# Optimization experiments

Hardware: AMD Instinct MI355X
Metric: run time of the kernel (lower is better)

## Reference

```python
import jax, jax.numpy as jnp
import numpy as np
import math

S, B, D, H, NL, K = 64, 1024, 512, 8, 4, 32
DH = D // H
DFF = 4 * D


def _pe():
    # sinusoidal positional encoding, shape [S, 1, D], scaled by 1/sqrt(D)
    pos = np.arange(S, dtype=np.float32)[:, None]
    div = np.exp(np.arange(0, D, 2, dtype=np.float32) * (-math.log(10000.0) / D))
    pe = np.zeros((S, D), dtype=np.float32)
    pe[:, 0::2] = np.sin(pos * div)
    pe[:, 1::2] = np.cos(pos * div)
    return jnp.asarray(pe[:, None, :] / math.sqrt(D))


def _ln(x, g, b, eps=1e-5):
    m = jnp.mean(x, axis=-1, keepdims=True)
    v = jnp.mean(jnp.square(x - m), axis=-1, keepdims=True)
    return (x - m) * jax.lax.rsqrt(v + eps) * g + b


def setup_inputs() -> dict:
    key = jax.random.key(0)
    ks = jax.random.split(key, 16)
    s = 0.02
    return {
        "x": jax.random.normal(ks[0], (S, B, D), dtype=jnp.float32),
        "ln1_g": jnp.ones((NL, D), jnp.float32),
        "ln1_b": jnp.zeros((NL, D), jnp.float32),
        "qkv_w": jax.random.normal(ks[1], (NL, 3 * D, D), jnp.float32) * s,
        "qkv_b": jnp.zeros((NL, 3 * D), jnp.float32),
        "out_w": jax.random.normal(ks[2], (NL, D, D), jnp.float32) * s,
        "out_b": jnp.zeros((NL, D), jnp.float32),
        "ln2_g": jnp.ones((NL, D), jnp.float32),
        "ln2_b": jnp.zeros((NL, D), jnp.float32),
        "mlp_w1": jax.random.normal(ks[3], (NL, DFF, D), jnp.float32) * s,
        "mlp_b1": jnp.zeros((NL, DFF), jnp.float32),
        "mlp_w2": jax.random.normal(ks[4], (NL, D, DFF), jnp.float32) * s,
        "mlp_b2": jnp.zeros((NL, D), jnp.float32),
        "hash_w": jax.random.normal(ks[5], (K, D), jnp.float32) * s,
        "hash_b": jnp.zeros((K,), jnp.float32),
    }


def reference(x, ln1_g, ln1_b, qkv_w, qkv_b, out_w, out_b,
              ln2_g, ln2_b, mlp_w1, mlp_b1, mlp_w2, mlp_b2,
              hash_w, hash_b):
    # positional encoding (dropout p=0.0 is identity)
    x = x + _pe()
    scale = 1.0 / math.sqrt(DH)
    for i in range(NL):
        # pre-LN multi-head self-attention
        h = _ln(x, ln1_g[i], ln1_b[i])
        qkv = h @ qkv_w[i].T + qkv_b[i]                      # [S,B,3D]
        q, k, v = jnp.split(qkv, 3, axis=-1)
        q = q.reshape(S, B, H, DH)
        k = k.reshape(S, B, H, DH)
        v = v.reshape(S, B, H, DH)
        scores = jnp.einsum('sbhd,tbhd->bhst', q, k) * scale  # [B,H,S,S]
        attn = jax.nn.softmax(scores, axis=-1)
        o = jnp.einsum('bhst,tbhd->sbhd', attn, v).reshape(S, B, D)
        x = x + o @ out_w[i].T + out_b[i]
        # pre-LN MLP with QuickGELU
        h = _ln(x, ln2_g[i], ln2_b[i])
        h1 = h @ mlp_w1[i].T + mlp_b1[i]
        h1 = h1 * jax.nn.sigmoid(1.702 * h1)
        x = x + h1 @ mlp_w2[i].T + mlp_b2[i]
    # BitwiseHashing: per-bit Linear(D,1) applied per seq position, mean over S,
    # concat over k bits, tanh -> equals tanh(mean_S(x) @ W^T + b)
    pooled = jnp.mean(x, axis=0)                              # [B,D]
    return jnp.tanh(pooled @ hash_w.T + hash_b)               # [B,K]
```

## Files before the change

### kernel.cpp

```cpp
#include <hip/hip_runtime.h>
#include <hip/hip_bf16.h>
#include <math.h>

#define S_   64
#define B_   1024
#define D_   512
#define H_   8
#define NL_  4
#define DH_  64
#define DFF_ 2048
#define NTOK (S_*B_)

typedef __bf16 bf16;
typedef __bf16 bf16x8 __attribute__((ext_vector_type(8)));
typedef float  f32x4  __attribute__((ext_vector_type(4)));

#define AS1(p) ((__attribute__((address_space(1))) void*)(void*)(p))
#define AS3(p) ((__attribute__((address_space(3))) void*)(p))

__global__ __launch_bounds__(256) void cvt_k(const float* __restrict__ s,
                                             bf16* __restrict__ d, int n) {
    int i = (blockIdx.x * 256 + threadIdx.x) * 4;
    if (i < n) {
        float4 v = *(const float4*)(s + i);
        bf16 o4[4] = {(bf16)v.x, (bf16)v.y, (bf16)v.z, (bf16)v.w};
        *(ushort4*)(d + i) = *(const ushort4*)o4;
    }
}

__global__ __launch_bounds__(256) void pe_add_k(const float* __restrict__ x,
                                                float* __restrict__ X) {
    int id = blockIdx.x * 256 + threadIdx.x;
    int n = id >> 8;
    int j = id & 255;
    int s = n >> 10;
    float div = expf((float)j * -0.03597789207803197f);
    float ang = (float)s * div;
    const float inv = 0.04419417382415922f;
    float2 v = *(const float2*)(x + (long)n * 512 + 2 * j);
    v.x += sinf(ang) * inv;
    v.y += cosf(ang) * inv;
    *(float2*)(X + (long)n * 512 + 2 * j) = v;
}

__global__ __launch_bounds__(256) void ln_k(const float* __restrict__ X,
                                            const float* __restrict__ g,
                                            const float* __restrict__ be,
                                            bf16* __restrict__ out) {
    long row = (long)blockIdx.x * 4 + (threadIdx.x >> 6);
    int lane = threadIdx.x & 63;
    const float* xr = X + row * 512 + lane * 8;
    float4 v0 = *(const float4*)xr;
    float4 v1 = *(const float4*)(xr + 4);
    float vv[8] = {v0.x, v0.y, v0.z, v0.w, v1.x, v1.y, v1.z, v1.w};
    float s = 0.f, sq = 0.f;
    #pragma unroll
    for (int j = 0; j < 8; j++) { s += vv[j]; sq += vv[j] * vv[j]; }
    #pragma unroll
    for (int off = 1; off < 64; off <<= 1) {
        s  += __shfl_xor(s, off);
        sq += __shfl_xor(sq, off);
    }
    float mean = s * (1.f / 512.f);
    float var  = sq * (1.f / 512.f) - mean * mean;
    float rs = rsqrtf(var + 1e-5f);
    int d = lane * 8;
    bf16 o8[8];
    #pragma unroll
    for (int j = 0; j < 8; j++)
        o8[j] = (bf16)((vv[j] - mean) * rs * g[d + j] + be[d + j]);
    *(uint4*)(out + row * 512 + d) = *(const uint4*)o8;
}

template<int EPI>
__global__ __launch_bounds__(256)
void gemm_bt(const bf16* __restrict__ A, const bf16* __restrict__ Bw,
             const float* __restrict__ bias, float* __restrict__ Xres,
             bf16* __restrict__ Obf, int Mdim, int K) {
    __shared__ bf16 As[128 * 32];
    __shared__ bf16 Bs[128 * 32];
    const int tid  = threadIdx.x;
    const int lane = tid & 63;
    const int wave = tid >> 6;
    const long rowBlk = (long)blockIdx.y * 128;
    const long colBlk = (long)blockIdx.x * 128;

    const int c0 = tid;
    const bf16* ag0 = A  + (rowBlk + (c0 >> 2)) * K + (c0 & 3) * 8;
    const bf16* ag1 = ag0 + 64 * (long)K;
    const bf16* bg0 = Bw + (colBlk + (c0 >> 2)) * K + (c0 & 3) * 8;
    const bf16* bg1 = bg0 + 64 * (long)K;
    bf16* al0 = As + c0 * 8;
    bf16* al1 = As + (c0 + 256) * 8;
    bf16* bl0 = Bs + c0 * 8;
    bf16* bl1 = Bs + (c0 + 256) * 8;

    const int wm = (wave >> 1) * 64, wn = (wave & 1) * 64;
    const int lr = lane & 15, lq = lane >> 4;

    f32x4 acc[4][4] = {};

    for (int k0 = 0; k0 < K; k0 += 32) {
        __builtin_amdgcn_global_load_lds(AS1(ag0 + k0), AS3(al0), 16, 0, 0);
        __builtin_amdgcn_global_load_lds(AS1(ag1 + k0), AS3(al1), 16, 0, 0);
        __builtin_amdgcn_global_load_lds(AS1(bg0 + k0), AS3(bl0), 16, 0, 0);
        __builtin_amdgcn_global_load_lds(AS1(bg1 + k0), AS3(bl1), 16, 0, 0);
        __syncthreads();
        bf16x8 af[4], bfr[4];
        #pragma unroll
        for (int mi = 0; mi < 4; mi++)
            af[mi] = *(const bf16x8*)(As + (wm + mi * 16 + lr) * 32 + lq * 8);
        #pragma unroll
        for (int ni = 0; ni < 4; ni++)
            bfr[ni] = *(const bf16x8*)(Bs + (wn + ni * 16 + lr) * 32 + lq * 8);
        #pragma unroll
        for (int mi = 0; mi < 4; mi++)
            #pragma unroll
            for (int ni = 0; ni < 4; ni++)
                acc[mi][ni] = __builtin_amdgcn_mfma_f32_16x16x32_bf16(
                    af[mi], bfr[ni], acc[mi][ni], 0, 0, 0);
        __syncthreads();
    }

    #pragma unroll
    for (int mi = 0; mi < 4; mi++) {
        #pragma unroll
        for (int ni = 0; ni < 4; ni++) {
            #pragma unroll
            for (int r = 0; r < 4; r++) {
                long row = rowBlk + wm + mi * 16 + lq * 4 + r;
                long col = colBlk + wn + ni * 16 + lr;
                float v = acc[mi][ni][r] + bias[col];
                if (EPI == 0) {
                    Obf[row * Mdim + col] = (bf16)v;
                } else {
                    Xres[row * Mdim + col] += v;
                }
            }
        }
    }
}

__global__ __launch_bounds__(256, 2)
void fused_mlp(const bf16* __restrict__ A,
               const bf16* __restrict__ W1,
               const float* __restrict__ b1,
               const bf16* __restrict__ W2,
               const float* __restrict__ b2,
               float* __restrict__ X) {
    __shared__ bf16 As[64 * 128];
    __shared__ bf16 Ws[16384];
    __shared__ bf16 h1s[64 * 136];
    const int tid = threadIdx.x;
    const int lane = tid & 63;
    const int w = tid >> 6;
    const int lr = lane & 15, lq = lane >> 4;
    const long rowBlk = (long)blockIdx.x * 64;

    f32x4 acc2[4][8] = {};

    for (int j = 0; j < 16; j++) {
        f32x4 acc1[4][2] = {};
        for (int kk = 0; kk < 4; kk++) {
            #pragma unroll
            for (int r = 0; r < 4; r++) {
                int c = tid + r * 256;
                int row = c >> 4, ks = c & 15;
                int ko = ks ^ (row & 7);
                __builtin_amdgcn_global_load_lds(
                    AS1(A + (rowBlk + row) * 512 + kk * 128 + ko * 8),
                    AS3(As + c * 8), 16, 0, 0);
            }
            #pragma unroll
            for (int r = 0; r < 8; r++) {
                int c = tid + r * 256;
                int n = c >> 4, ks = c & 15;
                int ko = ks ^ (n & 7);
                __builtin_amdgcn_global_load_lds(
                    AS1(W1 + ((long)j * 128 + n) * 512 + kk * 128 + ko * 8),
                    AS3(Ws + c * 8), 16, 0, 0);
            }
            __syncthreads();
            #pragma unroll
            for (int kh = 0; kh < 4; kh++) {
                bf16x8 af[4], bfx[2];
                #pragma unroll
                for (int ri = 0; ri < 4; ri++) {
                    int row = ri * 16 + lr;
                    int ks = (kh * 4 + lq) ^ (row & 7);
                    af[ri] = *(const bf16x8*)(As + row * 128 + ks * 8);
                }
                #pragma unroll
                for (int ci = 0; ci < 2; ci++) {
                    int n = w * 32 + ci * 16 + lr;
                    int ks = (kh * 4 + lq) ^ (n & 7);
                    bfx[ci] = *(const bf16x8*)(Ws + n * 128 + ks * 8);
                }
                #pragma unroll
                for (int ri = 0; ri < 4; ri++)
                    #pragma unroll
                    for (int ci = 0; ci < 2; ci++)
                        acc1[ri][ci] = __builtin_amdgcn_mfma_f32_16x16x32_bf16(
                            af[ri], bfx[ci], acc1[ri][ci], 0, 0, 0);
            }
            __syncthreads();
        }
        #pragma unroll
        for (int ci = 0; ci < 2; ci++) {
            int col = w * 32 + ci * 16 + lr;
            float bv = b1[j * 128 + col];
            #pragma unroll
            for (int ri = 0; ri < 4; ri++) {
                #pragma unroll
                for (int r = 0; r < 4; r++) {
                    int row = ri * 16 + lq * 4 + r;
                    float v = acc1[ri][ci][r] + bv;
                    float g = v / (1.f + __expf(-1.702f * v));
                    h1s[row * 136 + col] = (bf16)g;
                }
            }
        }
        __syncthreads();
        for (int kk2 = 0; kk2 < 4; kk2++) {
            #pragma unroll
            for (int r = 0; r < 8; r++) {
                int c = tid + r * 256;
                int n = c >> 2, ks = c & 3;
                int ko = ks ^ ((n >> 1) & 3);
                __builtin_amdgcn_global_load_lds(
                    AS1(W2 + (long)n * 2048 + j * 128 + kk2 * 32 + ko * 8),
                    AS3(Ws + c * 8), 16, 0, 0);
            }
            __syncthreads();
            bf16x8 af2[4], bf2[8];
            #pragma unroll
            for (int ri = 0; ri < 4; ri++)
                af2[ri] = *(const bf16x8*)(h1s + (ri * 16 + lr) * 136 + kk2 * 32 + lq * 8);
            #pragma unroll
            for (int ci = 0; ci < 8; ci++) {
                int n = w * 128 + ci * 16 + lr;
                int ks = lq ^ ((n >> 1) & 3);
                bf2[ci] = *(const bf16x8*)(Ws + n * 32 + ks * 8);
            }
            #pragma unroll
            for (int ri = 0; ri < 4; ri++)
                #pragma unroll
                for (int ci = 0; ci < 8; ci++)
                    acc2[ri][ci] = __builtin_amdgcn_mfma_f32_16x16x32_bf16(
                        af2[ri], bf2[ci], acc2[ri][ci], 0, 0, 0);
            __syncthreads();
        }
    }
    #pragma unroll
    for (int ci = 0; ci < 8; ci++) {
        int col = w * 128 + ci * 16 + lr;
        float bv = b2[col];
        #pragma unroll
        for (int ri = 0; ri < 4; ri++) {
            #pragma unroll
            for (int r = 0; r < 4; r++) {
                long row = rowBlk + ri * 16 + lq * 4 + r;
                X[row * 512 + col] += acc2[ri][ci][r] + bv;
            }
        }
    }
}

__global__ __launch_bounds__(256)
void attn_k(const bf16* __restrict__ qkv, bf16* __restrict__ o) {
    __shared__ bf16 qs[64 * 64], ks[64 * 64], vts[64 * 64], ps[64 * 64];
    const int tid = threadIdx.x;
    const int b = blockIdx.x >> 3;
    const int h = blockIdx.x & 7;
    const int lane = tid & 63;
    const int w = tid >> 6;

    #pragma unroll
    for (int half = 0; half < 2; half++) {
        int c = tid + half * 256;
        int trow = c >> 3;
        int off = (c & 7) * 8;
        const bf16* base = qkv + ((long)(trow * B_ + b)) * 1536 + h * 64 + off;
        *(uint4*)(qs + trow * 64 + off) = *(const uint4*)(base);
        *(uint4*)(ks + trow * 64 + off) = *(const uint4*)(base + 512);
        uint4 vv = *(const uint4*)(base + 1024);
        bf16 vtmp[8];
        *(uint4*)vtmp = vv;
        #pragma unroll
        for (int j = 0; j < 8; j++) vts[(off + j) * 64 + trow] = vtmp[j];
    }
    __syncthreads();

    const int lr = lane & 15, lq = lane >> 4;

    f32x4 sc[4] = {};
    #pragma unroll
    for (int d0 = 0; d0 < 64; d0 += 32) {
        bf16x8 aq = *(const bf16x8*)(qs + (w * 16 + lr) * 64 + d0 + lq * 8);
        #pragma unroll
        for (int ni = 0; ni < 4; ni++) {
            bf16x8 bk = *(const bf16x8*)(ks + (ni * 16 + lr) * 64 + d0 + lq * 8);
            sc[ni] = __builtin_amdgcn_mfma_f32_16x16x32_bf16(aq, bk, sc[ni], 0, 0, 0);
        }
    }
    float p[4][4];
    #pragma unroll
    for (int r = 0; r < 4; r++) {
        float m = -1e30f;
        #pragma unroll
        for (int ni = 0; ni < 4; ni++) { sc[ni][r] *= 0.125f; m = fmaxf(m, sc[ni][r]); }
        #pragma unroll
        for (int off = 1; off < 16; off <<= 1) m = fmaxf(m, __shfl_xor(m, off));
        float sum = 0.f;
        #pragma unroll
        for (int ni = 0; ni < 4; ni++) { p[ni][r] = __expf(sc[ni][r] - m); sum += p[ni][r]; }
        #pragma unroll
        for (int off = 1; off < 16; off <<= 1) sum += __shfl_xor(sum, off);
        float inv = 1.f / sum;
        #pragma unroll
        for (int ni = 0; ni < 4; ni++)
            ps[(w * 16 + lq * 4 + r) * 64 + ni * 16 + lr] = (bf16)(p[ni][r] * inv);
    }
    __syncthreads();

    f32x4 oa[4] = {};
    #pragma unroll
    for (int t0 = 0; t0 < 64; t0 += 32) {
        bf16x8 ap = *(const bf16x8*)(ps + (w * 16 + lr) * 64 + t0 + lq * 8);
        #pragma unroll
        for (int ni = 0; ni < 4; ni++) {
            bf16x8 bv = *(const bf16x8*)(vts + (ni * 16 + lr) * 64 + t0 + lq * 8);
            oa[ni] = __builtin_amdgcn_mfma_f32_16x16x32_bf16(ap, bv, oa[ni], 0, 0, 0);
        }
    }
    #pragma unroll
    for (int ni = 0; ni < 4; ni++) {
        #pragma unroll
        for (int r = 0; r < 4; r++) {
            int s = w * 16 + lq * 4 + r;
            int d = ni * 16 + lr;
            o[((long)(s * B_ + b)) * 512 + h * 64 + d] = (bf16)oa[ni][r];
        }
    }
}

__global__ __launch_bounds__(256)
void poolhash_k(const float* __restrict__ X, const float* __restrict__ hw,
                const float* __restrict__ hb, float* __restrict__ out) {
    __shared__ float pooled[512];
    __shared__ float part[8][32];
    int b = blockIdx.x, tid = threadIdx.x;
    for (int d = tid; d < 512; d += 256) {
        float acc = 0.f;
        #pragma unroll 8
        for (int s = 0; s < 64; s++) acc += X[((long)(s * B_ + b)) * 512 + d];
        pooled[d] = acc * (1.f / 64.f);
    }
    __syncthreads();
    int k = tid & 31, ch = tid >> 5;
    float p = 0.f;
    for (int d = ch * 64; d < ch * 64 + 64; d++) p += pooled[d] * hw[k * 512 + d];
    part[ch][k] = p;
    __syncthreads();
    if (tid < 32) {
        float t = hb[tid];
        #pragma unroll
        for (int c = 0; c < 8; c++) t += part[c][tid];
        out[b * 32 + tid] = tanhf(t);
    }
}

extern "C" void kernel_launch(void* const* d_in, const int* in_sizes, int n_in,
                              void* d_out, int out_size, void* d_ws, size_t ws_size,
                              hipStream_t stream) {
    const float* x      = (const float*)d_in[0];
    const float* ln1_g  = (const float*)d_in[1];
    const float* ln1_b  = (const float*)d_in[2];
    const float* qkv_w  = (const float*)d_in[3];
    const float* qkv_b  = (const float*)d_in[4];
    const float* out_w  = (const float*)d_in[5];
    const float* out_b  = (const float*)d_in[6];
    const float* ln2_g  = (const float*)d_in[7];
    const float* ln2_b  = (const float*)d_in[8];
    const float* mlp_w1 = (const float*)d_in[9];
    const float* mlp_b1 = (const float*)d_in[10];
    const float* mlp_w2 = (const float*)d_in[11];
    const float* mlp_b2 = (const float*)d_in[12];
    const float* hash_w = (const float*)d_in[13];
    const float* hash_b = (const float*)d_in[14];

    char* ws = (char*)d_ws;
    float* X  = (float*)ws;
    bf16* BIG = (bf16*)(ws + 134217728);
    bf16* Hb  = (bf16*)(ws + 134217728 + 268435456);
    size_t wo = 134217728 + 268435456 + 67108864;
    bf16* Wq = (bf16*)(ws + wo);            wo += (size_t)NL_ * 1536 * 512 * 2;
    bf16* Wo = (bf16*)(ws + wo);            wo += (size_t)NL_ * 512 * 512 * 2;
    bf16* W1 = (bf16*)(ws + wo);            wo += (size_t)NL_ * 2048 * 512 * 2;
    bf16* W2 = (bf16*)(ws + wo);            wo += (size_t)NL_ * 512 * 2048 * 2;

    cvt_k<<<(NL_ * 1536 * 512) / 1024, 256, 0, stream>>>(qkv_w,  Wq, NL_ * 1536 * 512);
    cvt_k<<<(NL_ * 512  * 512) / 1024, 256, 0, stream>>>(out_w,  Wo, NL_ * 512  * 512);
    cvt_k<<<(NL_ * 2048 * 512) / 1024, 256, 0, stream>>>(mlp_w1, W1, NL_ * 2048 * 512);
    cvt_k<<<(NL_ * 512 * 2048) / 1024, 256, 0, stream>>>(mlp_w2, W2, NL_ * 512 * 2048);

    pe_add_k<<<(NTOK * 256) / 256, 256, 0, stream>>>(x, X);

    for (int i = 0; i < NL_; i++) {
        ln_k<<<NTOK / 4, 256, 0, stream>>>(X, ln1_g + i * 512, ln1_b + i * 512, Hb);
        gemm_bt<0><<<dim3(12, 512), 256, 0, stream>>>(Hb, Wq + (size_t)i * 1536 * 512,
                                                      qkv_b + i * 1536, nullptr, BIG, 1536, 512);
        attn_k<<<B_ * H_, 256, 0, stream>>>(BIG, Hb);
        gemm_bt<2><<<dim3(4, 512), 256, 0, stream>>>(Hb, Wo + (size_t)i * 512 * 512,
                                                     out_b + i * 512, X, nullptr, 512, 512);
        ln_k<<<NTOK / 4, 256, 0, stream>>>(X, ln2_g + i * 512, ln2_b + i * 512, Hb);
        fused_mlp<<<NTOK / 64, 256, 0, stream>>>(Hb, W1 + (size_t)i * 2048 * 512,
                                                 mlp_b1 + i * 2048,
                                                 W2 + (size_t)i * 512 * 2048,
                                                 mlp_b2 + i * 512, X);
    }

    poolhash_k<<<B_, 256, 0, stream>>>(X, hash_w, hash_b, (float*)d_out);
}
```

Measured before the change: 3.742 ms.

## Split fused MLP over 8 waves and alias A and h1 LDS buffers

The fused MLP kernel moves from 4 to 8 waves per block. Each wave now owns a 2x2 tile of the first GEMM and a 64-column slice of the second GEMM, which halves the per-thread accumulator state. The A-tile and h1 staging buffers share one LDS region, cutting LDS per block and removing one barrier. The aim is higher occupancy and more latency hiding. The aggressive launch bound (512 threads, 4 blocks) may force the compiler to cap registers, which risks spills, and LDS capacity may still limit resident blocks.

```diff
diff --git a/kernel.cpp b/kernel.cpp
--- a/kernel.cpp
+++ b/kernel.cpp
@@ -141,39 +141,39 @@
     }
 }
 
-__global__ __launch_bounds__(256, 2)
+__global__ __launch_bounds__(512, 4)
 void fused_mlp(const bf16* __restrict__ A,
                const bf16* __restrict__ W1,
                const float* __restrict__ b1,
                const bf16* __restrict__ W2,
                const float* __restrict__ b2,
                float* __restrict__ X) {
-    __shared__ bf16 As[64 * 128];
+    __shared__ bf16 U[8704];
     __shared__ bf16 Ws[16384];
-    __shared__ bf16 h1s[64 * 136];
     const int tid = threadIdx.x;
     const int lane = tid & 63;
     const int w = tid >> 6;
     const int lr = lane & 15, lq = lane >> 4;
     const long rowBlk = (long)blockIdx.x * 64;
-
-    f32x4 acc2[4][8] = {};
+    const int mh = w & 1, nq = w >> 1;
+
+    f32x4 acc2[4][4] = {};
 
     for (int j = 0; j < 16; j++) {
-        f32x4 acc1[4][2] = {};
+        f32x4 acc1[2][2] = {};
         for (int kk = 0; kk < 4; kk++) {
             #pragma unroll
-            for (int r = 0; r < 4; r++) {
-                int c = tid + r * 256;
+            for (int r = 0; r < 2; r++) {
+                int c = tid + r * 512;
                 int row = c >> 4, ks = c & 15;
                 int ko = ks ^ (row & 7);
                 __builtin_amdgcn_global_load_lds(
                     AS1(A + (rowBlk + row) * 512 + kk * 128 + ko * 8),
-                    AS3(As + c * 8), 16, 0, 0);
-            }
-            #pragma unroll
-            for (int r = 0; r < 8; r++) {
-                int c = tid + r * 256;
+                    AS3(U + c * 8), 16, 0, 0);
+            }
+            #pragma unroll
+            for (int r = 0; r < 4; r++) {
+                int c = tid + r * 512;
                 int n = c >> 4, ks = c & 15;
                 int ko = ks ^ (n & 7);
                 __builtin_amdgcn_global_load_lds(
@@ -183,48 +183,46 @@
             __syncthreads();
             #pragma unroll
             for (int kh = 0; kh < 4; kh++) {
-                bf16x8 af[4], bfx[2];
+                int g = kh * 4 + lq;
+                bf16x8 af[2], bfx[2];
                 #pragma unroll
-                for (int ri = 0; ri < 4; ri++) {
-                    int row = ri * 16 + lr;
-                    int ks = (kh * 4 + lq) ^ (row & 7);
-                    af[ri] = *(const bf16x8*)(As + row * 128 + ks * 8);
+                for (int mi = 0; mi < 2; mi++) {
+                    int row = mh * 32 + mi * 16 + lr;
+                    af[mi] = *(const bf16x8*)(U + row * 128 + (g ^ (row & 7)) * 8);
                 }
                 #pragma unroll
-                for (int ci = 0; ci < 2; ci++) {
-                    int n = w * 32 + ci * 16 + lr;
-                    int ks = (kh * 4 + lq) ^ (n & 7);
-                    bfx[ci] = *(const bf16x8*)(Ws + n * 128 + ks * 8);
+                for (int ni = 0; ni < 2; ni++) {
+                    int n = nq * 32 + ni * 16 + lr;
+                    bfx[ni] = *(const bf16x8*)(Ws + n * 128 + (g ^ (n & 7)) * 8);
                 }
                 #pragma unroll
-                for (int ri = 0; ri < 4; ri++)
+                for (int mi = 0; mi < 2; mi++)
                     #pragma unroll
-                    for (int ci = 0; ci < 2; ci++)
-                        acc1[ri][ci] = __builtin_amdgcn_mfma_f32_16x16x32_bf16(
-                            af[ri], bfx[ci], acc1[ri][ci], 0, 0, 0);
+                    for (int ni = 0; ni < 2; ni++)
+                        acc1[mi][ni] = __builtin_amdgcn_mfma_f32_16x16x32_bf16(
+                            af[mi], bfx[ni], acc1[mi][ni], 0, 0, 0);
             }
             __syncthreads();
         }
         #pragma unroll
-        for (int ci = 0; ci < 2; ci++) {
-            int col = w * 32 + ci * 16 + lr;
+        for (int ni = 0; ni < 2; ni++) {
+            int col = nq * 32 + ni * 16 + lr;
             float bv = b1[j * 128 + col];
             #pragma unroll
-            for (int ri = 0; ri < 4; ri++) {
+            for (int mi = 0; mi < 2; mi++) {
                 #pragma unroll
                 for (int r = 0; r < 4; r++) {
-                    int row = ri * 16 + lq * 4 + r;
-                    float v = acc1[ri][ci][r] + bv;
-                    float g = v / (1.f + __expf(-1.702f * v));
-                    h1s[row * 136 + col] = (bf16)g;
+                    int row = mh * 32 + mi * 16 + lq * 4 + r;
+                    float v = acc1[mi][ni][r] + bv;
+                    float gv = v / (1.f + __expf(-1.702f * v));
+                    U[row * 136 + col] = (bf16)gv;
                 }
             }
         }
-        __syncthreads();
         for (int kk2 = 0; kk2 < 4; kk2++) {
             #pragma unroll
-            for (int r = 0; r < 8; r++) {
-                int c = tid + r * 256;
+            for (int r = 0; r < 4; r++) {
+                int c = tid + r * 512;
                 int n = c >> 2, ks = c & 3;
                 int ko = ks ^ ((n >> 1) & 3);
                 __builtin_amdgcn_global_load_lds(
@@ -232,35 +230,34 @@
                     AS3(Ws + c * 8), 16, 0, 0);
             }
             __syncthreads();
-            bf16x8 af2[4], bf2[8];
+            bf16x8 af2[4], bf2[4];
             #pragma unroll
             for (int ri = 0; ri < 4; ri++)
-                af2[ri] = *(const bf16x8*)(h1s + (ri * 16 + lr) * 136 + kk2 * 32 + lq * 8);
-            #pragma unroll
-            for (int ci = 0; ci < 8; ci++) {
-                int n = w * 128 + ci * 16 + lr;
-                int ks = lq ^ ((n >> 1) & 3);
-                bf2[ci] = *(const bf16x8*)(Ws + n * 32 + ks * 8);
+                af2[ri] = *(const bf16x8*)(U + (ri * 16 + lr) * 136 + kk2 * 32 + lq * 8);
+            #pragma unroll
+            for (int ni = 0; ni < 4; ni++) {
+                int n = w * 64 + ni * 16 + lr;
+                bf2[ni] = *(const bf16x8*)(Ws + n * 32 + ((lq ^ ((n >> 1) & 3))) * 8);
             }
             #pragma unroll
             for (int ri = 0; ri < 4; ri++)
                 #pragma unroll
-                for (int ci = 0; ci < 8; ci++)
-                    acc2[ri][ci] = __builtin_amdgcn_mfma_f32_16x16x32_bf16(
-                        af2[ri], bf2[ci], acc2[ri][ci], 0, 0, 0);
+                for (int ni = 0; ni < 4; ni++)
+                    acc2[ri][ni] = __builtin_amdgcn_mfma_f32_16x16x32_bf16(
+                        af2[ri], bf2[ni], acc2[ri][ni], 0, 0, 0);
             __syncthreads();
         }
     }
     #pragma unroll
-    for (int ci = 0; ci < 8; ci++) {
-        int col = w * 128 + ci * 16 + lr;
+    for (int ni = 0; ni < 4; ni++) {
+        int col = w * 64 + ni * 16 + lr;
         float bv = b2[col];
         #pragma unroll
         for (int ri = 0; ri < 4; ri++) {
             #pragma unroll
             for (int r = 0; r < 4; r++) {
                 long row = rowBlk + ri * 16 + lq * 4 + r;
-                X[row * 512 + col] += acc2[ri][ci][r] + bv;
+                X[row * 512 + col] += acc2[ri][ni][r] + bv;
             }
         }
     }
@@ -414,7 +411,7 @@
         gemm_bt<2><<<dim3(4, 512), 256, 0, stream>>>(Hb, Wo + (size_t)i * 512 * 512,
                                                      out_b + i * 512, X, nullptr, 512, 512);
         ln_k<<<NTOK / 4, 256, 0, stream>>>(X, ln2_g + i * 512, ln2_b + i * 512, Hb);
-        fused_mlp<<<NTOK / 64, 256, 0, stream>>>(Hb, W1 + (size_t)i * 2048 * 512,
+        fused_mlp<<<NTOK / 64, 512, 0, stream>>>(Hb, W1 + (size_t)i * 2048 * 512,
                                                  mlp_b1 + i * 2048,
                                                  W2 + (size_t)i * 512 * 2048,
                                                  mlp_b2 + i * 512, X);
```

Measured after the change: 4.192 ms. 1.12x slower.

## Double-buffer weights and switch fused MLP to 32x32x16 MFMA with fragment-ordered LDS

Applied to the files above, without the earlier changes.

Rewrites the fused MLP kernel to use 32x32x16 bf16 MFMA instead of 16x16x32, stages A, W1 and W2 into LDS in a fragment-native layout so each lane reads contiguous 16-byte chunks without swizzle math, and double-buffers the weight tiles so the next W1/W2 tile loads while the current one is multiplied. The h1 activation tile reuses the A staging buffer. The intent is to hide global-to-LDS latency and cut LDS read instructions per MFMA. In exchange, shared memory use and synchronisation ordering grow more complex, and the buffer reuse carries a risk of races.

```diff
diff --git a/kernel.cpp b/kernel.cpp
--- a/kernel.cpp
+++ b/kernel.cpp
@@ -14,6 +14,7 @@
 typedef __bf16 bf16;
 typedef __bf16 bf16x8 __attribute__((ext_vector_type(8)));
 typedef float  f32x4  __attribute__((ext_vector_type(4)));
+typedef float  f32x16 __attribute__((ext_vector_type(16)));
 
 #define AS1(p) ((__attribute__((address_space(1))) void*)(void*)(p))
 #define AS3(p) ((__attribute__((address_space(3))) void*)(p))
@@ -148,119 +149,132 @@
                const bf16* __restrict__ W2,
                const float* __restrict__ b2,
                float* __restrict__ X) {
-    __shared__ bf16 As[64 * 128];
-    __shared__ bf16 Ws[16384];
-    __shared__ bf16 h1s[64 * 136];
-    const int tid = threadIdx.x;
+    __shared__ bf16 U[8192];
+    __shared__ bf16 Wb[2][16384];
+    const int tid  = threadIdx.x;
     const int lane = tid & 63;
-    const int w = tid >> 6;
-    const int lr = lane & 15, lq = lane >> 4;
+    const int w    = tid >> 6;
+    const int lh   = lane >> 5;
+    const int l31  = lane & 31;
     const long rowBlk = (long)blockIdx.x * 64;
-
-    f32x4 acc2[4][8] = {};
+    const int mh    = w & 1;
+    const int cpair = (w >> 1) * 2;
+
+    auto stageA = [&](int kk) {
+        #pragma unroll
+        for (int r = 0; r < 4; r++) {
+            int c = tid + r * 256;
+            int mt = c >> 9, s = (c >> 6) & 7, l = c & 63;
+            __builtin_amdgcn_global_load_lds(
+                AS1(A + (rowBlk + mt * 32 + (l & 31)) * 512
+                      + kk * 128 + s * 16 + (l >> 5) * 8),
+                AS3(U + c * 8), 16, 0, 0);
+        }
+    };
+    auto stageW1 = [&](int j, int kk, int pb) {
+        #pragma unroll
+        for (int r = 0; r < 8; r++) {
+            int c = tid + r * 256;
+            int nt1 = c >> 9, s = (c >> 6) & 7, l = c & 63;
+            __builtin_amdgcn_global_load_lds(
+                AS1(W1 + ((long)j * 128 + nt1 * 32 + (l & 31)) * 512
+                      + kk * 128 + s * 16 + (l >> 5) * 8),
+                AS3(Wb[pb] + c * 8), 16, 0, 0);
+        }
+    };
+    auto stageW2 = [&](int j, int kk2, int pb) {
+        #pragma unroll
+        for (int r = 0; r < 8; r++) {
+            int c = tid + r * 256;
+            int nt = c >> 7, s3 = (c >> 6) & 1, l = c & 63;
+            __builtin_amdgcn_global_load_lds(
+                AS1(W2 + ((long)(nt * 32 + (l & 31))) * 2048
+                      + j * 128 + kk2 * 32 + s3 * 16 + (l >> 5) * 8),
+                AS3(Wb[pb] + c * 8), 16, 0, 0);
+        }
+    };
+
+    f32x16 acc2[2][4] = {};
+
+    stageW1(0, 0, 0);
 
     for (int j = 0; j < 16; j++) {
-        f32x4 acc1[4][2] = {};
+        f32x16 acc1[2] = {};
         for (int kk = 0; kk < 4; kk++) {
-            #pragma unroll
-            for (int r = 0; r < 4; r++) {
-                int c = tid + r * 256;
-                int row = c >> 4, ks = c & 15;
-                int ko = ks ^ (row & 7);
-                __builtin_amdgcn_global_load_lds(
-                    AS1(A + (rowBlk + row) * 512 + kk * 128 + ko * 8),
-                    AS3(As + c * 8), 16, 0, 0);
-            }
-            #pragma unroll
-            for (int r = 0; r < 8; r++) {
-                int c = tid + r * 256;
-                int n = c >> 4, ks = c & 15;
-                int ko = ks ^ (n & 7);
-                __builtin_amdgcn_global_load_lds(
-                    AS1(W1 + ((long)j * 128 + n) * 512 + kk * 128 + ko * 8),
-                    AS3(Ws + c * 8), 16, 0, 0);
-            }
             __syncthreads();
-            #pragma unroll
-            for (int kh = 0; kh < 4; kh++) {
-                bf16x8 af[4], bfx[2];
+            stageA(kk);
+            __syncthreads();
+            if (kk < 3) stageW1(j, kk + 1, (kk + 1) & 1);
+            else        stageW2(j, 0, 0);
+            const bf16* Wp = Wb[kk & 1];
+            #pragma unroll
+            for (int s = 0; s < 8; s++) {
+                bf16x8 af = *(const bf16x8*)(U + ((mh * 8 + s) * 64 + lane) * 8);
                 #pragma unroll
-                for (int ri = 0; ri < 4; ri++) {
-                    int row = ri * 16 + lr;
-                    int ks = (kh * 4 + lq) ^ (row & 7);
-                    af[ri] = *(const bf16x8*)(As + row * 128 + ks * 8);
+                for (int ct = 0; ct < 2; ct++) {
+                    bf16x8 bfr = *(const bf16x8*)
+                        (Wp + (((cpair + ct) * 8 + s) * 64 + lane) * 8);
+                    acc1[ct] = __builtin_amdgcn_mfma_f32_32x32x16_bf16(
+                        af, bfr, acc1[ct], 0, 0, 0);
                 }
-                #pragma unroll
-                for (int ci = 0; ci < 2; ci++) {
-                    int n = w * 32 + ci * 16 + lr;
-                    int ks = (kh * 4 + lq) ^ (n & 7);
-                    bfx[ci] = *(const bf16x8*)(Ws + n * 128 + ks * 8);
-                }
-                #pragma unroll
-                for (int ri = 0; ri < 4; ri++)
-                    #pragma unroll
-                    for (int ci = 0; ci < 2; ci++)
-                        acc1[ri][ci] = __builtin_amdgcn_mfma_f32_16x16x32_bf16(
-                            af[ri], bfx[ci], acc1[ri][ci], 0, 0, 0);
-            }
-            __syncthreads();
-        }
-        #pragma unroll
-        for (int ci = 0; ci < 2; ci++) {
-            int col = w * 32 + ci * 16 + lr;
-            float bv = b1[j * 128 + col];
-            #pragma unroll
-            for (int ri = 0; ri < 4; ri++) {
-                #pragma unroll
-                for (int r = 0; r < 4; r++) {
-                    int row = ri * 16 + lq * 4 + r;
-                    float v = acc1[ri][ci][r] + bv;
-                    float g = v / (1.f + __expf(-1.702f * v));
-                    h1s[row * 136 + col] = (bf16)g;
-                }
-            }
-        }
+            }
+        }
+        __syncthreads();
+        #pragma unroll
+        for (int ct = 0; ct < 2; ct++) {
+            int colg = (cpair + ct) * 32 + l31;
+            float b1v = b1[j * 128 + colg];
+            bf16* dst = U + (mh * 8 + (colg >> 4)) * 512
+                          + ((colg >> 3) & 1) * 256 + (colg & 7);
+            #pragma unroll
+            for (int r = 0; r < 16; r++) {
+                int rowin = (r & 3) + 8 * (r >> 2) + 4 * lh;
+                float v = acc1[ct][r] + b1v;
+                float gv = v / (1.f + __expf(-1.702f * v));
+                dst[rowin * 8] = (bf16)gv;
+            }
+        }
+        stageW2(j, 1, 1);
         __syncthreads();
         for (int kk2 = 0; kk2 < 4; kk2++) {
-            #pragma unroll
-            for (int r = 0; r < 8; r++) {
-                int c = tid + r * 256;
-                int n = c >> 2, ks = c & 3;
-                int ko = ks ^ ((n >> 1) & 3);
-                __builtin_amdgcn_global_load_lds(
-                    AS1(W2 + (long)n * 2048 + j * 128 + kk2 * 32 + ko * 8),
-                    AS3(Ws + c * 8), 16, 0, 0);
-            }
-            __syncthreads();
-            bf16x8 af2[4], bf2[8];
-            #pragma unroll
-            for (int ri = 0; ri < 4; ri++)
-                af2[ri] = *(const bf16x8*)(h1s + (ri * 16 + lr) * 136 + kk2 * 32 + lq * 8);
-            #pragma unroll
-            for (int ci = 0; ci < 8; ci++) {
-                int n = w * 128 + ci * 16 + lr;
-                int ks = lq ^ ((n >> 1) & 3);
-                bf2[ci] = *(const bf16x8*)(Ws + n * 32 + ks * 8);
-            }
-            #pragma unroll
-            for (int ri = 0; ri < 4; ri++)
+            const bf16* Wp = Wb[kk2 & 1];
+            #pragma unroll
+            for (int s3 = 0; s3 < 2; s3++) {
+                int sblk = kk2 * 2 + s3;
+                bf16x8 af2[2], bf2[4];
                 #pragma unroll
-                for (int ci = 0; ci < 8; ci++)
-                    acc2[ri][ci] = __builtin_amdgcn_mfma_f32_16x16x32_bf16(
-                        af2[ri], bf2[ci], acc2[ri][ci], 0, 0, 0);
-            __syncthreads();
-        }
-    }
-    #pragma unroll
-    for (int ci = 0; ci < 8; ci++) {
-        int col = w * 128 + ci * 16 + lr;
+                for (int m2 = 0; m2 < 2; m2++)
+                    af2[m2] = *(const bf16x8*)
+                        (U + ((m2 * 8 + sblk) * 64 + lane) * 8);
+                #pragma unroll
+                for (int ci = 0; ci < 4; ci++)
+                    bf2[ci] = *(const bf16x8*)
+                        (Wp + (((w * 4 + ci) * 2 + s3) * 64 + lane) * 8);
+                #pragma unroll
+                for (int m2 = 0; m2 < 2; m2++)
+                    #pragma unroll
+                    for (int ci = 0; ci < 4; ci++)
+                        acc2[m2][ci] = __builtin_amdgcn_mfma_f32_32x32x16_bf16(
+                            af2[m2], bf2[ci], acc2[m2][ci], 0, 0, 0);
+            }
+            if (kk2 < 3) {
+                __syncthreads();
+                if      (kk2 == 0) stageW2(j, 2, 0);
+                else if (kk2 == 1) stageW2(j, 3, 1);
+                else if (j < 15)   stageW1(j + 1, 0, 0);
+            }
+        }
+    }
+    #pragma unroll
+    for (int ci = 0; ci < 4; ci++) {
+        int col = w * 128 + ci * 32 + l31;
         float bv = b2[col];
         #pragma unroll
-        for (int ri = 0; ri < 4; ri++) {
-            #pragma unroll
-            for (int r = 0; r < 4; r++) {
-                long row = rowBlk + ri * 16 + lq * 4 + r;
-                X[row * 512 + col] += acc2[ri][ci][r] + bv;
+        for (int m2 = 0; m2 < 2; m2++) {
+            #pragma unroll
+            for (int r = 0; r < 16; r++) {
+                long row = rowBlk + m2 * 32 + (r & 3) + 8 * (r >> 2) + 4 * lh;
+                X[row * 512 + col] += acc2[m2][ci][r] + bv;
             }
         }
     }
```

Result: slower. 5.533 ms (+47.8%).

## Double-buffer fused MLP LDS tiles to overlap global loads with MFMA

Applied to the files above, without the earlier changes.

Restructures the fused MLP kernel to use two LDS buffers with smaller K chunks (64 for GEMM1, half-N chunks for GEMM2), prefetching the next stage's tiles, including across the GEMM1/GEMM2 boundary and into the next j iteration, while computing on the current one. This removes the load-then-sync stall at each K step. It also remaps the W2 column assignment so each wave covers interleaved 16-column groups. Halving the chunk size doubles the number of barriers, and the LDS footprint stays about the same, so occupancy should be unchanged.

```diff
diff --git a/kernel.cpp b/kernel.cpp
--- a/kernel.cpp
+++ b/kernel.cpp
@@ -148,53 +148,72 @@
                const bf16* __restrict__ W2,
                const float* __restrict__ b2,
                float* __restrict__ X) {
-    __shared__ bf16 As[64 * 128];
-    __shared__ bf16 Ws[16384];
+    __shared__ bf16 As[2][4096];
+    __shared__ bf16 Ws[2][8192];
     __shared__ bf16 h1s[64 * 136];
-    const int tid = threadIdx.x;
+    const int tid  = threadIdx.x;
     const int lane = tid & 63;
-    const int w = tid >> 6;
+    const int w    = tid >> 6;
     const int lr = lane & 15, lq = lane >> 4;
     const long rowBlk = (long)blockIdx.x * 64;
 
+    auto stage1 = [&](int j, int c, int pb) {
+        #pragma unroll
+        for (int r = 0; r < 2; r++) {
+            int cc = tid + r * 256;
+            int row = cc >> 3, ks = cc & 7;
+            int ko = ks ^ (row & 7);
+            __builtin_amdgcn_global_load_lds(
+                AS1(A + (rowBlk + row) * 512 + c * 64 + ko * 8),
+                AS3(As[pb] + cc * 8), 16, 0, 0);
+        }
+        #pragma unroll
+        for (int r = 0; r < 4; r++) {
+            int cc = tid + r * 256;
+            int n = cc >> 3, ks = cc & 7;
+            int ko = ks ^ (n & 7);
+            __builtin_amdgcn_global_load_lds(
+                AS1(W1 + ((long)j * 128 + n) * 512 + c * 64 + ko * 8),
+                AS3(Ws[pb] + cc * 8), 16, 0, 0);
+        }
+    };
+    auto stage2 = [&](int j, int c, int pb) {
+        int kc = c >> 1, nh = c & 1;
+        #pragma unroll
+        for (int r = 0; r < 4; r++) {
+            int cc = tid + r * 256;
+            int n = cc >> 2, ks = cc & 3;
+            int ko = ks ^ ((n >> 1) & 3);
+            __builtin_amdgcn_global_load_lds(
+                AS1(W2 + ((long)(nh * 256 + n)) * 2048 + j * 128 + kc * 32 + ko * 8),
+                AS3(Ws[pb] + cc * 8), 16, 0, 0);
+        }
+    };
+
     f32x4 acc2[4][8] = {};
+
+    stage1(0, 0, 0);
+    __syncthreads();
 
     for (int j = 0; j < 16; j++) {
         f32x4 acc1[4][2] = {};
-        for (int kk = 0; kk < 4; kk++) {
-            #pragma unroll
-            for (int r = 0; r < 4; r++) {
-                int c = tid + r * 256;
-                int row = c >> 4, ks = c & 15;
-                int ko = ks ^ (row & 7);
-                __builtin_amdgcn_global_load_lds(
-                    AS1(A + (rowBlk + row) * 512 + kk * 128 + ko * 8),
-                    AS3(As + c * 8), 16, 0, 0);
-            }
-            #pragma unroll
-            for (int r = 0; r < 8; r++) {
-                int c = tid + r * 256;
-                int n = c >> 4, ks = c & 15;
-                int ko = ks ^ (n & 7);
-                __builtin_amdgcn_global_load_lds(
-                    AS1(W1 + ((long)j * 128 + n) * 512 + kk * 128 + ko * 8),
-                    AS3(Ws + c * 8), 16, 0, 0);
-            }
-            __syncthreads();
-            #pragma unroll
-            for (int kh = 0; kh < 4; kh++) {
+        for (int c = 0; c < 8; c++) {
+            int pb = c & 1;
+            if (c < 7) stage1(j, c + 1, pb ^ 1);
+            else       stage2(j, 0, pb ^ 1);
+            #pragma unroll
+            for (int kh = 0; kh < 2; kh++) {
+                int g = kh * 4 + lq;
                 bf16x8 af[4], bfx[2];
                 #pragma unroll
                 for (int ri = 0; ri < 4; ri++) {
                     int row = ri * 16 + lr;
-                    int ks = (kh * 4 + lq) ^ (row & 7);
-                    af[ri] = *(const bf16x8*)(As + row * 128 + ks * 8);
+                    af[ri] = *(const bf16x8*)(As[pb] + row * 64 + (g ^ (row & 7)) * 8);
                 }
                 #pragma unroll
                 for (int ci = 0; ci < 2; ci++) {
                     int n = w * 32 + ci * 16 + lr;
-                    int ks = (kh * 4 + lq) ^ (n & 7);
-                    bfx[ci] = *(const bf16x8*)(Ws + n * 128 + ks * 8);
+                    bfx[ci] = *(const bf16x8*)(Ws[pb] + n * 64 + (g ^ (n & 7)) * 8);
                 }
                 #pragma unroll
                 for (int ri = 0; ri < 4; ri++)
@@ -215,52 +234,48 @@
                 for (int r = 0; r < 4; r++) {
                     int row = ri * 16 + lq * 4 + r;
                     float v = acc1[ri][ci][r] + bv;
-                    float g = v / (1.f + __expf(-1.702f * v));
-                    h1s[row * 136 + col] = (bf16)g;
+                    float gv = v / (1.f + __expf(-1.702f * v));
+                    h1s[row * 136 + col] = (bf16)gv;
                 }
             }
         }
         __syncthreads();
-        for (int kk2 = 0; kk2 < 4; kk2++) {
-            #pragma unroll
-            for (int r = 0; r < 8; r++) {
-                int c = tid + r * 256;
-                int n = c >> 2, ks = c & 3;
-                int ko = ks ^ ((n >> 1) & 3);
-                __builtin_amdgcn_global_load_lds(
-                    AS1(W2 + (long)n * 2048 + j * 128 + kk2 * 32 + ko * 8),
-                    AS3(Ws + c * 8), 16, 0, 0);
+        for (int c = 0; c < 8; c++) {
+            int pb = c & 1;
+            if (c < 7)          stage2(j, c + 1, pb ^ 1);
+            else if (j < 15)    stage1(j + 1, 0, pb ^ 1);
+            int kc = c >> 1, nh = c & 1;
+            bf16x8 af2[4], bf2[4];
+            #pragma unroll
+            for (int ri = 0; ri < 4; ri++)
+                af2[ri] = *(const bf16x8*)(h1s + (ri * 16 + lr) * 136 + kc * 32 + lq * 8);
+            #pragma unroll
+            for (int t = 0; t < 4; t++) {
+                int n = (t * 4 + w) * 16 + lr;
+                bf2[t] = *(const bf16x8*)(Ws[pb] + n * 32 + ((lq ^ ((n >> 1) & 3))) * 8);
             }
+            #pragma unroll
+            for (int ri = 0; ri < 4; ri++)
+                #pragma unroll
+                for (int t = 0; t < 4; t++)
+                    acc2[ri][nh * 4 + t] = __builtin_amdgcn_mfma_f32_16x16x32_bf16(
+                        af2[ri], bf2[t], acc2[ri][nh * 4 + t], 0, 0, 0);
             __syncthreads();
-            bf16x8 af2[4], bf2[8];
-            #pragma unroll
-            for (int ri = 0; ri < 4; ri++)
-                af2[ri] = *(const bf16x8*)(h1s + (ri * 16 + lr) * 136 + kk2 * 32 + lq * 8);
-            #pragma unroll
-            for (int ci = 0; ci < 8; ci++) {
-                int n = w * 128 + ci * 16 + lr;
-                int ks = lq ^ ((n >> 1) & 3);
-                bf2[ci] = *(const bf16x8*)(Ws + n * 32 + ks * 8);
-            }
-            #pragma unroll
-            for (int ri = 0; ri < 4; ri++)
-                #pragma unroll
-                for (int ci = 0; ci < 8; ci++)
-                    acc2[ri][ci] = __builtin_amdgcn_mfma_f32_16x16x32_bf16(
-                        af2[ri], bf2[ci], acc2[ri][ci], 0, 0, 0);
-            __syncthreads();
-        }
-    }
-    #pragma unroll
-    for (int ci = 0; ci < 8; ci++) {
-        int col = w * 128 + ci * 16 + lr;
-        float bv = b2[col];
-        #pragma unroll
-        for (int ri = 0; ri < 4; ri++) {
-            #pragma unroll
-            for (int r = 0; r < 4; r++) {
-                long row = rowBlk + ri * 16 + lq * 4 + r;
-                X[row * 512 + col] += acc2[ri][ci][r] + bv;
+        }
+    }
+    #pragma unroll
+    for (int nh = 0; nh < 2; nh++) {
+        #pragma unroll
+        for (int t = 0; t < 4; t++) {
+            int col = nh * 256 + (t * 4 + w) * 16 + lr;
+            float bv = b2[col];
+            #pragma unroll
+            for (int ri = 0; ri < 4; ri++) {
+                #pragma unroll
+                for (int r = 0; r < 4; r++) {
+                    long row = rowBlk + ri * 16 + lq * 4 + r;
+                    X[row * 512 + col] += acc2[ri][nh * 4 + t][r] + bv;
+                }
             }
         }
     }
```

Result: slower. 4.414 ms (+17.9%).
